# Performance work log

Measured on AMD Instinct MI355X. Metric: run time of the kernel, lower is better.

The kernel has to match this reference:

```python
import jax, jax.numpy as jnp
import numpy as np

# ---- static config (matches init_kwargs) ----
B, SX, SY, SZ = 1, 64, 64, 64
W = 32            # HIDDEN_DIM
L = 4             # num_fourier_layers
M1 = M2 = M3 = 8  # fourier modes per axis
PX = PY = PZ = 8  # domain padding
ALPHA = 0.05      # leaky relu slope
OUTC = 6


def conv3d(x, w, pad):
    # x: (B,C,D,H,W), w: (O,I,kd,kh,kw)
    return jax.lax.conv_general_dilated(
        x, w, window_strides=(1, 1, 1), padding=[(pad, pad)] * 3,
        dimension_numbers=('NCDHW', 'OIDHW', 'NCDHW'))


def pad1(x):
    # periodic=(0,0,0) -> zero pad 1 on every spatial side (matches ZeroPad3d chain)
    return jnp.pad(x, ((0, 0), (0, 0), (1, 1), (1, 1), (1, 1)))


def basic_block(x, w1, w2):
    # BasicBlock3D_Periodic with use_shortcut=False
    out = jax.nn.leaky_relu(conv3d(pad1(x), w1, 0), ALPHA)
    return conv3d(pad1(out), w2, 0)


def spec_apply(xft_slice, w):
    # xft_slice: complex (B,C,d1,d2,d3); w: (2C,2C,5,5,5)
    re_im = jnp.concatenate([xft_slice.real, xft_slice.imag], axis=1)  # (B,2C,...)
    out = conv3d(re_im, w, 2)                                          # (B,2C,...)
    b, c2, d1, d2, d3 = out.shape
    out = out.reshape(b, c2 // 2, 2, d1, d2, d3)
    return jax.lax.complex(out[:, :, 0], out[:, :, 1])


def spectral_conv(x, ws):
    # ws: (8, 2W, 2W, 5, 5, 5); mode-limited per-octant conv in frequency space
    b, c, n, m, l = x.shape
    xft = jnp.fft.rfftn(x, axes=(-3, -2, -1))  # (b,c,n,m,l//2+1) complex
    out = jnp.zeros((b, c, n, m, l // 2 + 1), dtype=xft.dtype)
    octs = [
        (slice(None, M1),  slice(None, M2)),
        (slice(n - M1, None), slice(None, M2)),
        (slice(None, M1),  slice(m - M2, None)),
        (slice(n - M1, None), slice(m - M2, None)),
        (slice(M1, n - M1), slice(None, M2)),
        (slice(None, M1),  slice(M2, m - M2)),
        (slice(M1, n - M1), slice(m - M2, None)),
        (slice(n - M1, None), slice(M2, m - M2)),
    ]
    for i, (s1, s2) in enumerate(octs):
        out = out.at[:, :, s1, s2, :M3].set(spec_apply(xft[:, :, s1, s2, :M3], ws[i]))
    return jnp.fft.irfftn(out, s=(n, m, l), axes=(-3, -2, -1))


def setup_inputs() -> dict:
    key = jax.random.key(0)
    ks = jax.random.split(key, 16)
    f32 = jnp.float32
    d = {
        'yeex': jax.random.normal(ks[0], (B, SX, SY, SZ), f32),
        'yeey': jax.random.normal(ks[1], (B, SX, SY, SZ), f32),
        'yeez': jax.random.normal(ks[2], (B, SX, SY, SZ), f32),
        'fc0_w': jax.random.normal(ks[3], (6, W), f32) * 0.1,
        'fc0_b': jax.random.normal(ks[4], (W,), f32) * 0.01,
        'spec_w': jax.random.normal(ks[5], (L, 8, 2 * W, 2 * W, 5, 5, 5), f32) * 0.02,
        'blk_w1': jax.random.normal(ks[6], (L, W, W, 3, 3, 3), f32) * 0.05,
        'blk_w2': jax.random.normal(ks[7], (L, W, W, 3, 3, 3), f32) * 0.05,
        'fc1_w': jax.random.normal(ks[8], (W, 128), f32) * 0.05,
        'fc1_b': jax.random.normal(ks[9], (128,), f32) * 0.01,
        'fc2_w': jax.random.normal(ks[10], (128, OUTC), f32) * 0.05,
        'fc2_b': jax.random.normal(ks[11], (OUTC,), f32) * 0.01,
    }
    return d


def reference(yeex, yeey, yeez, fc0_w, fc0_b, spec_w, blk_w1, blk_w2,
              fc1_w, fc1_b, fc2_w, fc2_b):
    b, sx, sy, sz = yeez.shape
    # normalized coordinate grid (3 channels), as in standard FNO get_grid
    gx = jnp.broadcast_to(jnp.linspace(0., 1., sx, dtype=yeex.dtype)[None, :, None, None], (b, sx, sy, sz))
    gy = jnp.broadcast_to(jnp.linspace(0., 1., sy, dtype=yeex.dtype)[None, None, :, None], (b, sx, sy, sz))
    gz = jnp.broadcast_to(jnp.linspace(0., 1., sz, dtype=yeex.dtype)[None, None, None, :], (b, sx, sy, sz))
    inp = jnp.stack([yeex, yeey, yeez, gx, gy, gz], axis=-1)  # (b,sx,sy,sz,6)

    x = inp @ fc0_w + fc0_b                      # lift: (b,sx,sy,sz,W)
    x = jnp.transpose(x, (0, 4, 1, 2, 3))        # (b,W,sx,sy,sz)
    x = jnp.pad(x, ((0, 0), (0, 0), (0, PX), (0, PY), (0, PZ)))

    for i in range(L):
        x1 = spectral_conv(x, spec_w[i])
        x2 = basic_block(x, blk_w1[i], blk_w2[i])
        x = x1 + x2 + x
        if i < L - 1:
            x = jax.nn.leaky_relu(x, ALPHA)

    x = x[:, :, :sx, :sy, :sz]                   # crop domain padding
    x = jnp.transpose(x, (0, 2, 3, 4, 1))        # (b,sx,sy,sz,W)
    x = jax.nn.leaky_relu(x @ fc1_w + fc1_b, ALPHA)
    return x @ fc2_w + fc2_b                     # (b,sx,sy,sz,OUTC)
```

## Files before the change

kernel.cpp:

```cpp
#include <hip/hip_runtime.h>
#include <math.h>

#define NS 72
#define NS2 (NS*NS)
#define NS3 (NS*NS*NS)
#define MZ 8
#define LALPHA 0.05f
#define CSCALE (1.0f/256.0f)

typedef _Float16 f16x8 __attribute__((ext_vector_type(8)));
typedef _Float16 f16x4 __attribute__((ext_vector_type(4)));
typedef float f32x4 __attribute__((ext_vector_type(4)));

__device__ __forceinline__ float leakyf(float v){ return v > 0.f ? v : LALPHA*v; }

__constant__ int c_RX0[8] = {0,64,0,64, 8,0,8,64};
__constant__ int c_RNX[8] = {8,8,8,8, 56,8,56,8};
__constant__ int c_RY0[8] = {0,0,64,64, 0,8,64,8};
__constant__ int c_RNY[8] = {8,8,8,8, 8,56,8,56};
__constant__ int c_Bbase[8] = {0,1728,3456,5184, 6912,15552,24192,32832};
__constant__ int c_BY[8]    = {12,12,12,12, 12,60,12,60};

__global__ void k_tw(float2* tw){
  int t = threadIdx.x;
  if (t < NS){
    double th = (2.0*M_PI/72.0)*(double)t;
    tw[t] = make_float2((float)cos(th), (float)sin(th));
  }
}

__global__ void k_fc0(const float* __restrict__ yx, const float* __restrict__ yy,
                      const float* __restrict__ yz, const float* __restrict__ w,
                      const float* __restrict__ b, float* __restrict__ X){
  int idx = blockIdx.x*256 + threadIdx.x;
  int z = idx % NS; int t = idx / NS; int y = t % NS; t /= NS; int x = t % NS; int c = t / NS;
  float v = 0.f;
  if (x < 64 && y < 64 && z < 64){
    int p = (x*64 + y)*64 + z;
    float i0 = yx[p], i1 = yy[p], i2 = yz[p];
    float gx = (float)x*(1.f/63.f), gy = (float)y*(1.f/63.f), gz = (float)z*(1.f/63.f);
    v = b[c] + i0*w[0*32+c] + i1*w[1*32+c] + i2*w[2*32+c]
             + gx*w[3*32+c] + gy*w[4*32+c] + gz*w[5*32+c];
  }
  X[idx] = v;
}

__global__ void k_zdft(const float* __restrict__ X, float2* __restrict__ A, const float2* __restrict__ tw){
  __shared__ float2 stw[NS];
  int tid = threadIdx.x;
  if (tid < NS) stw[tid] = tw[tid];
  __syncthreads();
  int f = blockIdx.x*256 + tid;
  const float* row = X + (size_t)f*NS;
  float ar[MZ], ai[MZ]; int tk[MZ];
  #pragma unroll
  for (int k=0;k<MZ;k++){ ar[k]=0.f; ai[k]=0.f; tk[k]=0; }
  for (int z=0; z<NS; z++){
    float v = row[z];
    #pragma unroll
    for (int k=0;k<MZ;k++){
      float2 w = stw[tk[k]];
      ar[k] += v*w.x;
      ai[k] -= v*w.y;
      tk[k] += k; if (tk[k] >= NS) tk[k] -= NS;
    }
  }
  float2* o = A + (size_t)f*MZ;
  #pragma unroll
  for (int k=0;k<MZ;k++) o[k] = make_float2(ar[k], ai[k]);
}

__global__ void k_ydft(const float2* __restrict__ A, float2* __restrict__ B, const float2* __restrict__ tw){
  __shared__ float2 stw[NS];
  int tid = threadIdx.x;
  if (tid < NS) stw[tid] = tw[tid];
  __syncthreads();
  int f = blockIdx.x*256 + tid;
  int ky = f % NS; int cx = f / NS;
  const float2* in = A + (size_t)cx*NS*MZ;
  float ar[MZ], ai[MZ];
  #pragma unroll
  for (int k=0;k<MZ;k++){ ar[k]=0.f; ai[k]=0.f; }
  int t = 0;
  for (int y=0;y<NS;y++){
    float2 w = stw[t]; t += ky; if (t>=NS) t-=NS;
    const float2* iy = in + y*MZ;
    #pragma unroll
    for (int k=0;k<MZ;k++){
      float2 v = iy[k];
      ar[k] += v.x*w.x + v.y*w.y;
      ai[k] += v.y*w.x - v.x*w.y;
    }
  }
  float2* o = B + (size_t)f*MZ;
  #pragma unroll
  for (int k=0;k<MZ;k++) o[k] = make_float2(ar[k], ai[k]);
}

__global__ void k_xdft(const float2* __restrict__ B, float2* __restrict__ C, const float2* __restrict__ tw){
  __shared__ float2 stw[NS];
  int tid = threadIdx.x;
  if (tid < NS) stw[tid] = tw[tid];
  __syncthreads();
  int f = blockIdx.x*256 + tid;
  int ky = f % NS; int t2 = f / NS; int kx = t2 % NS; int c = t2 / NS;
  const float2* in = B + ((size_t)c*NS2 + ky)*MZ;
  float ar[MZ], ai[MZ];
  #pragma unroll
  for (int k=0;k<MZ;k++){ ar[k]=0.f; ai[k]=0.f; }
  int t = 0;
  for (int x=0;x<NS;x++){
    float2 w = stw[t]; t += kx; if (t>=NS) t-=NS;
    const float2* ix = in + (size_t)x*NS*MZ;
    #pragma unroll
    for (int k=0;k<MZ;k++){
      float2 v = ix[k];
      ar[k] += v.x*w.x + v.y*w.y;
      ai[k] += v.y*w.x - v.x*w.y;
    }
  }
  float2* o = C + (size_t)f*MZ;
  #pragma unroll
  for (int k=0;k<MZ;k++) o[k] = make_float2(ar[k], ai[k]);
}

__global__ void k_wpackh(const float* __restrict__ W, _Float16* __restrict__ Ah){
  int e = blockIdx.x*256 + threadIdx.x;
  int i = e & 63; int o = (e>>6) & 63;
  int t2 = e >> 12; int tap = t2 % 125; int r = t2 / 125;
  const float* wr = W + (size_t)r*64*64*125;
  Ah[e] = (_Float16)wr[((size_t)(o*64 + (i&1)*32 + (i>>1)))*125 + tap];
}

__global__ void k_cpackh(const float2* __restrict__ C, _Float16* __restrict__ Bg){
  int g = blockIdx.x*256 + threadIdx.x;
  int ci = g & 31; int elem = g >> 5;
  int r = 0;
  #pragma unroll
  for (int k=1;k<8;k++) if (elem >= c_Bbase[k]) r = k;
  int el = elem - c_Bbase[r];
  int BY = c_BY[r];
  int q3 = el % 12; int tt = el / 12; int q2 = tt % BY; int q1 = tt / BY;
  int kxr = q1-2, kyr = q2-2, kzr = q3-2;
  float2 v = make_float2(0.f,0.f);
  if ((unsigned)kxr < (unsigned)c_RNX[r] && (unsigned)kyr < (unsigned)c_RNY[r] && (unsigned)kzr < 8u){
    v = C[(((size_t)ci*NS + (c_RX0[r]+kxr))*NS + (c_RY0[r]+kyr))*MZ + kzr];
  }
  _Float16* o = Bg + (size_t)elem*64 + 2*ci;
  o[0] = (_Float16)(v.x*CSCALE);
  o[1] = (_Float16)(v.y*CSCALE);
}

__global__ __launch_bounds__(64) void k_freqmfma(const _Float16* __restrict__ Ah,
                                                 const _Float16* __restrict__ Bg,
                                                 float* __restrict__ Pp){
  int gb = blockIdx.x;
  int ks = gb >> 8; int b = gb & 255;
  int r, til;
  if (b < 32){ r = b>>3; til = b&7; }
  else       { r = 4 + (b-32)/56; til = (b-32)%56; }
  int BY = c_BY[r];
  int q1, q2base;
  if (r==5 || r==7){ q1 = 2 + til/7; q2base = 2 + (til%7)*8; }
  else             { q1 = 2 + til;   q2base = 2; }
  int lane = threadIdx.x;
  int l15 = lane & 15, kg = lane >> 4;
  int q2l = q2base + (l15>>3), q3l = 2 + (l15&7);
  const _Float16* Ar = Ah + (size_t)r*125*4096;
  const _Float16* Br = Bg + (size_t)c_Bbase[r]*64;
  int lb = q2l*12 + q3l;
  f32x4 acc[4][4];
  f32x4 zz = {0.f,0.f,0.f,0.f};
  #pragma unroll
  for (int m=0;m<4;m++)
    #pragma unroll
    for (int n=0;n<4;n++) acc[m][n] = zz;
  int t0 = ks*16;
  int t1 = t0+16 < 125 ? t0+16 : 125;
  for (int tt=t0; tt<t1; tt++){
    int td = tt/25; int rm = tt - td*25; int th = rm/5; int tz = rm - th*5;
    const _Float16* At = Ar + tt*4096;
    f16x8 a[4][2];
    #pragma unroll
    for (int mt=0;mt<4;mt++){
      a[mt][0] = *(const f16x8*)(At + (mt*16+l15)*64 + kg*8);
      a[mt][1] = *(const f16x8*)(At + (mt*16+l15)*64 + 32 + kg*8);
    }
    int ebase = (q1 + td - 2)*BY*12 + lb + (th-2)*12 + (tz-2);
    f16x8 bf[4][2];
    #pragma unroll
    for (int nt=0;nt<4;nt++){
      const _Float16* bp = Br + (size_t)(ebase + nt*24)*64 + kg*8;
      bf[nt][0] = *(const f16x8*)(bp);
      bf[nt][1] = *(const f16x8*)(bp + 32);
    }
    #pragma unroll
    for (int mt=0;mt<4;mt++)
      #pragma unroll
      for (int nt=0;nt<4;nt++){
        acc[mt][nt] = __builtin_amdgcn_mfma_f32_16x16x32_f16(a[mt][0], bf[nt][0], acc[mt][nt],0,0,0);
        acc[mt][nt] = __builtin_amdgcn_mfma_f32_16x16x32_f16(a[mt][1], bf[nt][1], acc[mt][nt],0,0,0);
      }
  }
  float* base = Pp + (((size_t)ks*256 + b)*64 + lane)*64;
  #pragma unroll
  for (int mt=0;mt<4;mt++)
    #pragma unroll
    for (int nt=0;nt<4;nt++)
      *(f32x4*)(base + mt*16 + nt*4) = acc[mt][nt];
}

__global__ void k_fred(const float* __restrict__ Pp, float* __restrict__ Df){
  int t = blockIdx.x*256 + threadIdx.x;
  int mtnt = t & 15; int lane = (t>>4) & 63; int b = t >> 10;
  int mt = mtnt >> 2, nt = mtnt & 3;
  int r, til;
  if (b < 32){ r = b>>3; til = b&7; }
  else       { r = 4 + (b-32)/56; til = (b-32)%56; }
  int x0 = c_RX0[r], y0 = c_RY0[r];
  int q1, q2base;
  if (r==5 || r==7){ q1 = 2 + til/7; q2base = 2 + (til%7)*8; }
  else             { q1 = 2 + til;   q2base = 2; }
  int l15 = lane & 15, kg = lane >> 4;
  int q2l = q2base + (l15>>3), q3l = 2 + (l15&7);
  f32x4 s = {0.f,0.f,0.f,0.f};
  #pragma unroll
  for (int ks=0;ks<8;ks++){
    s += *(const f32x4*)(Pp + (((size_t)ks*256 + b)*64 + lane)*64 + mtnt*4);
  }
  int kx = x0 + q1 - 2;
  int kz = q3l - 2;
  int ky = y0 + q2l + nt*2 - 2;
  #pragma unroll
  for (int rg=0;rg<4;rg++){
    int o = mt*16 + kg*4 + rg;
    int co = o >> 1, reim = o & 1;
    Df[((((size_t)co*NS + kx)*NS + ky)*MZ + kz)*2 + reim] = s[rg]*256.0f;
  }
}

__global__ void k_invx(const float2* __restrict__ D, float2* __restrict__ E, const float2* __restrict__ tw){
  __shared__ float2 stw[NS];
  int tid = threadIdx.x;
  if (tid < NS) stw[tid] = tw[tid];
  __syncthreads();
  int f = blockIdx.x*256 + tid;
  int ky = f % NS; int t2 = f / NS; int x = t2 % NS; int c = t2 / NS;
  const float2* in = D + ((size_t)c*NS2 + ky)*MZ;
  float ar[MZ], ai[MZ];
  #pragma unroll
  for (int k=0;k<MZ;k++){ ar[k]=0.f; ai[k]=0.f; }
  int t = 0;
  for (int kx=0;kx<NS;kx++){
    float2 w = stw[t]; t += x; if (t>=NS) t-=NS;
    const float2* ix = in + (size_t)kx*NS*MZ;
    #pragma unroll
    for (int k=0;k<MZ;k++){
      float2 v = ix[k];
      ar[k] += v.x*w.x - v.y*w.y;
      ai[k] += v.x*w.y + v.y*w.x;
    }
  }
  float2* o = E + (size_t)f*MZ;
  #pragma unroll
  for (int k=0;k<MZ;k++) o[k] = make_float2(ar[k]*(1.f/72.f), ai[k]*(1.f/72.f));
}

__global__ void k_invyz(const float2* __restrict__ E, float* __restrict__ X1, const float2* __restrict__ tw){
  __shared__ float2 stw[NS];
  int tid = threadIdx.x;
  if (tid < NS) stw[tid] = tw[tid];
  __syncthreads();
  int f = blockIdx.x*256 + tid;
  int y = f % NS; int t2 = f / NS; int x = t2 % NS; int c = t2 / NS;
  const float2* in = E + ((size_t)c*NS + x)*NS*MZ;
  float ar[MZ], ai[MZ];
  #pragma unroll
  for (int k=0;k<MZ;k++){ ar[k]=0.f; ai[k]=0.f; }
  int t = 0;
  for (int ky=0;ky<NS;ky++){
    float2 w = stw[t]; t += y; if (t>=NS) t-=NS;
    const float2* ik = in + ky*MZ;
    #pragma unroll
    for (int k=0;k<MZ;k++){
      float2 v = ik[k];
      ar[k] += v.x*w.x - v.y*w.y;
      ai[k] += v.x*w.y + v.y*w.x;
    }
  }
  const float scale = 1.f/(72.f*72.f);
  float* o = X1 + (size_t)f*NS;
  int tk[MZ];
  #pragma unroll
  for (int k=0;k<MZ;k++) tk[k]=0;
  for (int z=0; z<NS; z++){
    float acc = ar[0];
    #pragma unroll
    for (int k=1;k<MZ;k++){
      float2 w = stw[tk[k]];
      acc += 2.f*(ar[k]*w.x - ai[k]*w.y);
      tk[k] += k; if (tk[k] >= NS) tk[k] -= NS;
    }
    o[z] = acc*scale;
  }
}


__global__ void k_wcvt2(const float* __restrict__ w1, const float* __restrict__ w2,
                        _Float16* __restrict__ WhA, _Float16* __restrict__ WhB){
  int e = blockIdx.x*256 + threadIdx.x;
  int h = e >= 27648; int e2 = e - (h ? 27648 : 0);
  int tap = e2 >> 10; int co = (e2>>5)&31; int ci = e2&31;
  const float* w = h ? w2 : w1;
  _Float16* o = h ? WhB : WhA;
  o[e2] = (_Float16)w[(co*32+ci)*27 + tap];
}

__global__ void k_cvt16(const float* __restrict__ Xf, _Float16* __restrict__ Xg){
  int b = blockIdx.x;
  int tid = threadIdx.x;
  if (b >= 1458){
    _Float16* g = (b==1458) ? (Xg - 4096) : (Xg + (size_t)NS3*32);
    f16x8 zz = {0,0,0,0,0,0,0,0};
    f16x8* gp = (f16x8*)g;
    gp[tid] = zz; gp[tid+256] = zz;
    return;
  }
  int p = b*256 + tid;
  f16x8 o0,o1,o2,o3;
  #pragma unroll
  for (int c=0;c<8;c++){
    o0[c] = (_Float16)Xf[(size_t)c*NS3 + p];
    o1[c] = (_Float16)Xf[(size_t)(c+8)*NS3 + p];
    o2[c] = (_Float16)Xf[(size_t)(c+16)*NS3 + p];
    o3[c] = (_Float16)Xf[(size_t)(c+24)*NS3 + p];
  }
  f16x8* op = (f16x8*)(Xg + (size_t)p*32);
  op[0]=o0; op[1]=o1; op[2]=o2; op[3]=o3;
}

__global__ void k_zgH(_Float16* __restrict__ Hg){
  int e = blockIdx.x*256 + threadIdx.x;
  _Float16* g = (e < 512) ? (Hg - 4096 + e*8)
                          : (Hg + (size_t)NS3*32 + (size_t)(e-512)*8);
  f16x8 zz = {0,0,0,0,0,0,0,0};
  *(f16x8*)g = zz;
}

__global__ __launch_bounds__(256) void k_convm(const _Float16* __restrict__ Xg,
    const _Float16* __restrict__ Wh, float* __restrict__ OUT, _Float16* __restrict__ OUTH,
    const float* __restrict__ X1, const float* __restrict__ Xres,
    int mode2, int do_leaky){
  int tid = threadIdx.x;
  int orig = blockIdx.x;
  int xcd = orig & 7, loc = orig >> 3;
  int wg = (xcd < 2 ? xcd*183 : 366 + (xcd-2)*182) + loc;
  int j = wg*4 + (tid>>6);
  int slab = j/81, nb = j - slab*81;
  int q0 = nb*64;
  int lane = tid & 63;
  int l15 = lane & 15, kg = lane >> 4;
  f32x4 acc[2][4];
  f32x4 zz = {0.f,0.f,0.f,0.f};
  #pragma unroll
  for (int a=0;a<2;a++)
    #pragma unroll
    for (int b=0;b<4;b++) acc[a][b] = zz;
  for (int dx=0; dx<3; dx++){
    int xx = slab + dx - 1;
    if ((unsigned)xx >= 72u) continue;
    const _Float16* Xrow = Xg + ((size_t)xx*5184 + q0)*32;
    #pragma unroll
    for (int t9=0; t9<9; t9++){
      int tap = dx*9 + t9;
      int off = ((t9/3)-1)*72 + (t9%3) - 1;
      f16x8 a0 = *(const f16x8*)(Wh + ((tap*32 + l15)*32 + kg*8));
      f16x8 a1 = *(const f16x8*)(Wh + ((tap*32 + 16 + l15)*32 + kg*8));
      const _Float16* bbase = Xrow + (off + l15)*32 + kg*8;
      f16x8 b0 = *(const f16x8*)(bbase);
      f16x8 b1 = *(const f16x8*)(bbase + 512);
      f16x8 b2 = *(const f16x8*)(bbase + 1024);
      f16x8 b3 = *(const f16x8*)(bbase + 1536);
      acc[0][0] = __builtin_amdgcn_mfma_f32_16x16x32_f16(a0,b0,acc[0][0],0,0,0);
      acc[0][1] = __builtin_amdgcn_mfma_f32_16x16x32_f16(a0,b1,acc[0][1],0,0,0);
      acc[0][2] = __builtin_amdgcn_mfma_f32_16x16x32_f16(a0,b2,acc[0][2],0,0,0);
      acc[0][3] = __builtin_amdgcn_mfma_f32_16x16x32_f16(a0,b3,acc[0][3],0,0,0);
      acc[1][0] = __builtin_amdgcn_mfma_f32_16x16x32_f16(a1,b0,acc[1][0],0,0,0);
      acc[1][1] = __builtin_amdgcn_mfma_f32_16x16x32_f16(a1,b1,acc[1][1],0,0,0);
      acc[1][2] = __builtin_amdgcn_mfma_f32_16x16x32_f16(a1,b2,acc[1][2],0,0,0);
      acc[1][3] = __builtin_amdgcn_mfma_f32_16x16x32_f16(a1,b3,acc[1][3],0,0,0);
    }
  }
  if (mode2){
    #pragma unroll
    for (int nt=0; nt<4; nt++){
      int q = q0 + nt*16 + l15;
      int y = q/72, z = q - y*72;
      bool edge = (y==0)||(y==71)||(z==0)||(z==71);
      #pragma unroll
      for (int c2=0;c2<2;c2++){
        #pragma unroll
        for (int r=0;r<4;r++){
          int co = c2*16 + kg*4 + r;
          size_t idx = (size_t)co*NS3 + (size_t)slab*5184 + q;
          float v = acc[c2][nt][r];
          if (!edge){
            v += X1[idx] + Xres[idx];
            if (do_leaky) v = leakyf(v);
          }
          OUT[idx] = v;
        }
      }
    }
  } else {
    #pragma unroll
    for (int nt=0; nt<4; nt++){
      int q = q0 + nt*16 + l15;
      int y = q/72, z = q - y*72;
      bool edge = (y==0)||(y==71)||(z==0)||(z==71);
      _Float16* hp = OUTH + ((size_t)slab*5184 + q)*32 + kg*4;
      #pragma unroll
      for (int c2=0;c2<2;c2++){
        f32x4 av = acc[c2][nt];
        f16x4 hv;
        #pragma unroll
        for (int r=0;r<4;r++){
          float v = av[r];
          if (!edge) v = leakyf(v);
          hv[r] = (_Float16)v;
        }
        *(f16x4*)(hp + c2*16) = hv;
      }
    }
  }
}

__global__ void k_corrH(_Float16* __restrict__ H, const _Float16* __restrict__ Xg,
                        const _Float16* __restrict__ Wh){
  int t = blockIdx.x*256 + threadIdx.x;
  int co = t & 31; int t2 = t >> 5;
  int e = t2 % 284; int x = t2 / 284;
  int y, z;
  if (e < 72){ y = 0; z = e; }
  else if (e < 144){ y = 71; z = e - 72; }
  else if (e < 214){ z = 0; y = e - 143; }
  else { z = 71; y = e - 213; }
  int q = y*72 + z;
  float corr = 0.f;
  for (int tap=0; tap<27; tap++){
    int dx = tap/9, rr = tap%9, dy = rr/3, dz = rr%3;
    int xx = x + dx - 1;
    if ((unsigned)xx >= 72u) continue;
    int yy = y + dy - 1, zz = z + dz - 1;
    if ((unsigned)yy < 72u && (unsigned)zz < 72u) continue;
    int lin = (xx*5184 + q + (dy-1)*72 + (dz-1))*32;
    const _Float16* V = Xg + lin;
    const _Float16* Wr = Wh + (tap*32 + co)*32;
    float s = 0.f;
    #pragma unroll
    for (int ci=0; ci<32; ci++) s += (float)V[ci]*(float)Wr[ci];
    corr += s;
  }
  size_t idx = ((size_t)x*5184 + q)*32 + co;
  float v = (float)H[idx] - corr;
  v = leakyf(v);
  H[idx] = (_Float16)v;
}

__global__ void k_corr(float* __restrict__ OUT, const _Float16* __restrict__ Xg,
                       const _Float16* __restrict__ Wh, const float* __restrict__ X1,
                       const float* __restrict__ Xres, int mode2, int do_leaky){
  int t = blockIdx.x*256 + threadIdx.x;
  int co = t & 31; int t2 = t >> 5;
  int e = t2 % 284; int x = t2 / 284;
  int y, z;
  if (e < 72){ y = 0; z = e; }
  else if (e < 144){ y = 71; z = e - 72; }
  else if (e < 214){ z = 0; y = e - 143; }
  else { z = 71; y = e - 213; }
  int q = y*72 + z;
  float corr = 0.f;
  for (int tap=0; tap<27; tap++){
    int dx = tap/9, rr = tap%9, dy = rr/3, dz = rr%3;
    int xx = x + dx - 1;
    if ((unsigned)xx >= 72u) continue;
    int yy = y + dy - 1, zz = z + dz - 1;
    if ((unsigned)yy < 72u && (unsigned)zz < 72u) continue;
    int lin = (xx*5184 + q + (dy-1)*72 + (dz-1))*32;
    const _Float16* V = Xg + lin;
    const _Float16* Wr = Wh + (tap*32 + co)*32;
    float s = 0.f;
    #pragma unroll
    for (int ci=0; ci<32; ci++) s += (float)V[ci]*(float)Wr[ci];
    corr += s;
  }
  size_t idx = (size_t)co*NS3 + (size_t)x*5184 + q;
  float v = OUT[idx] - corr;
  if (mode2) v += X1[idx] + Xres[idx];
  if (do_leaky) v = leakyf(v);
  OUT[idx] = v;
}

__global__ void k_head(const float* __restrict__ X, const float* __restrict__ w1, const float* __restrict__ b1,
                       const float* __restrict__ w2, const float* __restrict__ b2, float* __restrict__ out){
  __shared__ float s1[32*128];
  __shared__ float sb1[128];
  __shared__ float s2[128*6];
  __shared__ float sb2[6];
  int tid = threadIdx.x;
  for (int e=tid;e<4096;e+=256) s1[e]=w1[e];
  if (tid<128) sb1[tid]=b1[tid];
  for (int e=tid;e<768;e+=256) s2[e]=w2[e];
  if (tid<6) sb2[tid]=b2[tid];
  __syncthreads();
  int p = blockIdx.x*256 + tid;
  int z = p % 64; int t = p / 64; int y = t % 64; int x = t / 64;
  size_t q = ((size_t)x*NS + y)*NS + z;
  float xin[32];
  #pragma unroll
  for (int c=0;c<32;c++) xin[c] = X[(size_t)c*NS3 + q];
  float acc[6];
  #pragma unroll
  for (int o=0;o<6;o++) acc[o]=sb2[o];
  for (int j=0;j<128;j++){
    float h = sb1[j];
    #pragma unroll
    for (int c=0;c<32;c++) h += xin[c]*s1[c*128+j];
    h = leakyf(h);
    #pragma unroll
    for (int o=0;o<6;o++) acc[o] += h*s2[j*6+o];
  }
  float* O = out + (size_t)p*6;
  #pragma unroll
  for (int o=0;o<6;o++) O[o]=acc[o];
}

extern "C" void kernel_launch(void* const* d_in, const int* in_sizes, int n_in,
                              void* d_out, int out_size, void* d_ws, size_t ws_size,
                              hipStream_t stream) {
  const float* yeex = (const float*)d_in[0];
  const float* yeey = (const float*)d_in[1];
  const float* yeez = (const float*)d_in[2];
  const float* fc0w = (const float*)d_in[3];
  const float* fc0b = (const float*)d_in[4];
  const float* specw= (const float*)d_in[5];
  const float* bw1  = (const float*)d_in[6];
  const float* bw2  = (const float*)d_in[7];
  const float* fc1w = (const float*)d_in[8];
  const float* fc1b = (const float*)d_in[9];
  const float* fc2w = (const float*)d_in[10];
  const float* fc2b = (const float*)d_in[11];
  float* out = (float*)d_out;
  float* ws  = (float*)d_ws;

  float*  P0 = ws;
  float*  X1 = ws + 11943936;
  float*  P2 = ws + 23887872;
  float2* A  = (float2*)(ws + 35831808);
  float2* B  = (float2*)(ws + 41140224);
  float2* Cf = (float2*)(ws + 46448640);
  float2* Df = (float2*)(ws + 51757056);
  float2* TW = (float2*)(ws + 57065472);
  _Float16* Ah = (_Float16*)A;
  _Float16* Bg = (_Float16*)B;
  float*    Pp = X1;
  _Float16* XhG = (_Float16*)(ws + 35831808) + 4096;
  _Float16* HhG = (_Float16*)(ws + 41807872) + 4096;
  _Float16* WhA = (_Float16*)(ws + 47783936);
  _Float16* WhB = (_Float16*)(ws + 47797760);

  float* curX = P0; float* curY = P2;

  k_tw<<<1,128,0,stream>>>(TW);
  k_fc0<<<46656,256,0,stream>>>(yeex,yeey,yeez,fc0w,fc0b,curX);
  for (int i=0;i<4;i++){
    k_zdft<<<648,256,0,stream>>>(curX, A, TW);
    k_ydft<<<648,256,0,stream>>>(A, B, TW);
    k_xdft<<<648,256,0,stream>>>(B, Cf, TW);
    k_wpackh<<<16000,256,0,stream>>>(specw + (size_t)i*8*64*64*125, Ah);
    k_cpackh<<<5184,256,0,stream>>>(Cf, Bg);
    hipMemsetAsync(Df, 0, (size_t)1327104*8, stream);
    k_freqmfma<<<2048,64,0,stream>>>(Ah, Bg, Pp);
    k_fred<<<1024,256,0,stream>>>(Pp, (float*)Df);
    k_invx<<<648,256,0,stream>>>(Df, A, TW);
    k_invyz<<<648,256,0,stream>>>(A, X1, TW);
    k_wcvt2<<<216,256,0,stream>>>(bw1 + (size_t)i*27648, bw2 + (size_t)i*27648, WhA, WhB);
    k_cvt16<<<1460,256,0,stream>>>(curX, XhG);
    k_zgH<<<4,256,0,stream>>>(HhG);
    k_convm<<<1458,256,0,stream>>>(XhG, WhA, nullptr, HhG, nullptr, nullptr, 0, 1);
    k_corrH<<<2556,256,0,stream>>>(HhG, XhG, WhA);
    k_convm<<<1458,256,0,stream>>>(HhG, WhB, curY, nullptr, X1, curX, 1, (i<3)?1:0);
    k_corr<<<2556,256,0,stream>>>(curY, HhG, WhB, X1, curX, 1, (i<3)?1:0);
    float* tmp = curX; curX = curY; curY = tmp;
  }
  k_head<<<1024,256,0,stream>>>(curX, fc1w, fc1b, fc2w, fc2b, out);
}
```

Measured before the change: 2.557 ms.

## Prune x-DFT to retained modes, store spectral output and residual in fp16, retile head

The x-axis DFT now computes only the frequency rows that the mode-limited spectral weights later read, split across two threads per output (four z-modes each). The spectral-branch output X1 is written as fp16, and the residual is read from the existing fp16 channel-last copy of the input instead of the fp32 tensor, which cuts epilogue memory traffic in the conv kernels. The head kernel handles two points per thread, reads transposed fc1 weights as float4 from LDS, and launches half as many blocks. Storing the spectral output and residual in fp16 lowers precision on the residual path, and the residual reads become strided across channels.

```diff
diff --git a/kernel.cpp b/kernel.cpp
--- a/kernel.cpp
+++ b/kernel.cpp
@@ -97,31 +97,38 @@
   for (int k=0;k<MZ;k++) o[k] = make_float2(ar[k], ai[k]);
 }
 
-__global__ void k_xdft(const float2* __restrict__ B, float2* __restrict__ C, const float2* __restrict__ tw){
+__global__ void k_xdftL(const float2* __restrict__ B, float2* __restrict__ C, const float2* __restrict__ tw){
   __shared__ float2 stw[NS];
   int tid = threadIdx.x;
   if (tid < NS) stw[tid] = tw[tid];
   __syncthreads();
-  int f = blockIdx.x*256 + tid;
-  int ky = f % NS; int t2 = f / NS; int kx = t2 % NS; int c = t2 / NS;
-  const float2* in = B + ((size_t)c*NS2 + ky)*MZ;
-  float ar[MZ], ai[MZ];
-  #pragma unroll
-  for (int k=0;k<MZ;k++){ ar[k]=0.f; ai[k]=0.f; }
-  int t = 0;
+  int t = blockIdx.x*256 + tid;
+  int h = t & 1; int t2 = t >> 1;
+  int c = t2 >> 11; int l = t2 & 2047;
+  int kx, ky;
+  if (l < 576){ ky = l & 7; kx = l >> 3; }
+  else if (l < 1152){ int e = l - 576; ky = 64 + (e & 7); kx = e >> 3; }
+  else { int e = l - 1152; int kyi = e >> 4; int kxi = e & 15;
+         ky = 8 + kyi; kx = (kxi < 8) ? kxi : 56 + kxi; }
+  int k0 = h*4;
+  const float2* in = B + ((size_t)c*NS2 + ky)*MZ + k0;
+  float ar[4], ai[4];
+  #pragma unroll
+  for (int k=0;k<4;k++){ ar[k]=0.f; ai[k]=0.f; }
+  int tt = 0;
   for (int x=0;x<NS;x++){
-    float2 w = stw[t]; t += kx; if (t>=NS) t-=NS;
+    float2 w = stw[tt]; tt += kx; if (tt>=NS) tt-=NS;
     const float2* ix = in + (size_t)x*NS*MZ;
     #pragma unroll
-    for (int k=0;k<MZ;k++){
+    for (int k=0;k<4;k++){
       float2 v = ix[k];
       ar[k] += v.x*w.x + v.y*w.y;
       ai[k] += v.y*w.x - v.x*w.y;
     }
   }
-  float2* o = C + (size_t)f*MZ;
-  #pragma unroll
-  for (int k=0;k<MZ;k++) o[k] = make_float2(ar[k], ai[k]);
+  float2* o = C + (((size_t)c*NS + kx)*NS + ky)*MZ + k0;
+  #pragma unroll
+  for (int k=0;k<4;k++) o[k] = make_float2(ar[k], ai[k]);
 }
 
 __global__ void k_wpackh(const float* __restrict__ W, _Float16* __restrict__ Ah){
@@ -266,7 +273,7 @@
   for (int k=0;k<MZ;k++) o[k] = make_float2(ar[k]*(1.f/72.f), ai[k]*(1.f/72.f));
 }
 
-__global__ void k_invyz(const float2* __restrict__ E, float* __restrict__ X1, const float2* __restrict__ tw){
+__global__ void k_invyz(const float2* __restrict__ E, _Float16* __restrict__ X1h, const float2* __restrict__ tw){
   __shared__ float2 stw[NS];
   int tid = threadIdx.x;
   if (tid < NS) stw[tid] = tw[tid];
@@ -289,7 +296,7 @@
     }
   }
   const float scale = 1.f/(72.f*72.f);
-  float* o = X1 + (size_t)f*NS;
+  _Float16* o = X1h + (size_t)f*NS;
   int tk[MZ];
   #pragma unroll
   for (int k=0;k<MZ;k++) tk[k]=0;
@@ -301,7 +308,7 @@
       acc += 2.f*(ar[k]*w.x - ai[k]*w.y);
       tk[k] += k; if (tk[k] >= NS) tk[k] -= NS;
     }
-    o[z] = acc*scale;
+    o[z] = (_Float16)(acc*scale);
   }
 }
 
@@ -349,7 +356,7 @@
 
 __global__ __launch_bounds__(256) void k_convm(const _Float16* __restrict__ Xg,
     const _Float16* __restrict__ Wh, float* __restrict__ OUT, _Float16* __restrict__ OUTH,
-    const float* __restrict__ X1, const float* __restrict__ Xres,
+    const _Float16* __restrict__ X1h, const _Float16* __restrict__ XresH,
     int mode2, int do_leaky){
   int tid = threadIdx.x;
   int orig = blockIdx.x;
@@ -405,7 +412,7 @@
           size_t idx = (size_t)co*NS3 + (size_t)slab*5184 + q;
           float v = acc[c2][nt][r];
           if (!edge){
-            v += X1[idx] + Xres[idx];
+            v += (float)X1h[idx] + (float)XresH[((size_t)slab*5184 + q)*32 + co];
             if (do_leaky) v = leakyf(v);
           }
           OUT[idx] = v;
@@ -468,8 +475,8 @@
 }
 
 __global__ void k_corr(float* __restrict__ OUT, const _Float16* __restrict__ Xg,
-                       const _Float16* __restrict__ Wh, const float* __restrict__ X1,
-                       const float* __restrict__ Xres, int mode2, int do_leaky){
+                       const _Float16* __restrict__ Wh, const _Float16* __restrict__ X1h,
+                       const _Float16* __restrict__ XresH, int mode2, int do_leaky){
   int t = blockIdx.x*256 + threadIdx.x;
   int co = t & 31; int t2 = t >> 5;
   int e = t2 % 284; int x = t2 / 284;
@@ -496,43 +503,60 @@
   }
   size_t idx = (size_t)co*NS3 + (size_t)x*5184 + q;
   float v = OUT[idx] - corr;
-  if (mode2) v += X1[idx] + Xres[idx];
+  if (mode2) v += (float)X1h[idx] + (float)XresH[((size_t)x*5184 + q)*32 + co];
   if (do_leaky) v = leakyf(v);
   OUT[idx] = v;
 }
 
 __global__ void k_head(const float* __restrict__ X, const float* __restrict__ w1, const float* __restrict__ b1,
                        const float* __restrict__ w2, const float* __restrict__ b2, float* __restrict__ out){
-  __shared__ float s1[32*128];
+  __shared__ float s1t[32*128];
   __shared__ float sb1[128];
   __shared__ float s2[128*6];
   __shared__ float sb2[6];
   int tid = threadIdx.x;
-  for (int e=tid;e<4096;e+=256) s1[e]=w1[e];
+  for (int e=tid;e<4096;e+=256){ int j=e>>5, c=e&31; s1t[e]=w1[c*128+j]; }
   if (tid<128) sb1[tid]=b1[tid];
   for (int e=tid;e<768;e+=256) s2[e]=w2[e];
   if (tid<6) sb2[tid]=b2[tid];
   __syncthreads();
-  int p = blockIdx.x*256 + tid;
-  int z = p % 64; int t = p / 64; int y = t % 64; int x = t / 64;
-  size_t q = ((size_t)x*NS + y)*NS + z;
-  float xin[32];
-  #pragma unroll
-  for (int c=0;c<32;c++) xin[c] = X[(size_t)c*NS3 + q];
-  float acc[6];
-  #pragma unroll
-  for (int o=0;o<6;o++) acc[o]=sb2[o];
+  int p0 = blockIdx.x*256 + tid;
+  float xin[2][32];
+  float acc[2][6];
+  #pragma unroll
+  for (int vv=0; vv<2; vv++){
+    int p = p0 + vv*131072;
+    int z = p % 64; int t = p / 64; int y = t % 64; int x = t / 64;
+    size_t q = ((size_t)x*NS + y)*NS + z;
+    #pragma unroll
+    for (int c=0;c<32;c++) xin[vv][c] = X[(size_t)c*NS3 + q];
+    #pragma unroll
+    for (int o=0;o<6;o++) acc[vv][o]=sb2[o];
+  }
   for (int j=0;j<128;j++){
-    float h = sb1[j];
-    #pragma unroll
-    for (int c=0;c<32;c++) h += xin[c]*s1[c*128+j];
-    h = leakyf(h);
-    #pragma unroll
-    for (int o=0;o<6;o++) acc[o] += h*s2[j*6+o];
-  }
-  float* O = out + (size_t)p*6;
-  #pragma unroll
-  for (int o=0;o<6;o++) O[o]=acc[o];
+    const float4* wj = (const float4*)(s1t + j*32);
+    float h0 = sb1[j], h1 = h0;
+    #pragma unroll
+    for (int c4=0;c4<8;c4++){
+      float4 w = wj[c4];
+      h0 += xin[0][c4*4+0]*w.x + xin[0][c4*4+1]*w.y + xin[0][c4*4+2]*w.z + xin[0][c4*4+3]*w.w;
+      h1 += xin[1][c4*4+0]*w.x + xin[1][c4*4+1]*w.y + xin[1][c4*4+2]*w.z + xin[1][c4*4+3]*w.w;
+    }
+    h0 = leakyf(h0); h1 = leakyf(h1);
+    const float* s2j = s2 + j*6;
+    #pragma unroll
+    for (int o=0;o<6;o++){
+      float wv = s2j[o];
+      acc[0][o] += h0*wv;
+      acc[1][o] += h1*wv;
+    }
+  }
+  #pragma unroll
+  for (int vv=0; vv<2; vv++){
+    float* O = out + (size_t)(p0 + vv*131072)*6;
+    #pragma unroll
+    for (int o=0;o<6;o++) O[o]=acc[vv][o];
+  }
 }
 
 extern "C" void kernel_launch(void* const* d_in, const int* in_sizes, int n_in,
@@ -554,7 +578,7 @@
   float* ws  = (float*)d_ws;
 
   float*  P0 = ws;
-  float*  X1 = ws + 11943936;
+  float*  X1s = ws + 11943936;
   float*  P2 = ws + 23887872;
   float2* A  = (float2*)(ws + 35831808);
   float2* B  = (float2*)(ws + 41140224);
@@ -563,7 +587,8 @@
   float2* TW = (float2*)(ws + 57065472);
   _Float16* Ah = (_Float16*)A;
   _Float16* Bg = (_Float16*)B;
-  float*    Pp = X1;
+  float*    Pp = X1s;
+  _Float16* X1h = (_Float16*)X1s;
   _Float16* XhG = (_Float16*)(ws + 35831808) + 4096;
   _Float16* HhG = (_Float16*)(ws + 41807872) + 4096;
   _Float16* WhA = (_Float16*)(ws + 47783936);
@@ -576,22 +601,22 @@
   for (int i=0;i<4;i++){
     k_zdft<<<648,256,0,stream>>>(curX, A, TW);
     k_ydft<<<648,256,0,stream>>>(A, B, TW);
-    k_xdft<<<648,256,0,stream>>>(B, Cf, TW);
+    k_xdftL<<<512,256,0,stream>>>(B, Cf, TW);
     k_wpackh<<<16000,256,0,stream>>>(specw + (size_t)i*8*64*64*125, Ah);
     k_cpackh<<<5184,256,0,stream>>>(Cf, Bg);
     hipMemsetAsync(Df, 0, (size_t)1327104*8, stream);
     k_freqmfma<<<2048,64,0,stream>>>(Ah, Bg, Pp);
     k_fred<<<1024,256,0,stream>>>(Pp, (float*)Df);
     k_invx<<<648,256,0,stream>>>(Df, A, TW);
-    k_invyz<<<648,256,0,stream>>>(A, X1, TW);
+    k_invyz<<<648,256,0,stream>>>(A, X1h, TW);
     k_wcvt2<<<216,256,0,stream>>>(bw1 + (size_t)i*27648, bw2 + (size_t)i*27648, WhA, WhB);
     k_cvt16<<<1460,256,0,stream>>>(curX, XhG);
     k_zgH<<<4,256,0,stream>>>(HhG);
     k_convm<<<1458,256,0,stream>>>(XhG, WhA, nullptr, HhG, nullptr, nullptr, 0, 1);
     k_corrH<<<2556,256,0,stream>>>(HhG, XhG, WhA);
-    k_convm<<<1458,256,0,stream>>>(HhG, WhB, curY, nullptr, X1, curX, 1, (i<3)?1:0);
-    k_corr<<<2556,256,0,stream>>>(curY, HhG, WhB, X1, curX, 1, (i<3)?1:0);
+    k_convm<<<1458,256,0,stream>>>(HhG, WhB, curY, nullptr, X1h, XhG, 1, (i<3)?1:0);
+    k_corr<<<2556,256,0,stream>>>(curY, HhG, WhB, X1h, XhG, 1, (i<3)?1:0);
     float* tmp = curX; curX = curY; curY = tmp;
   }
-  k_head<<<1024,256,0,stream>>>(curX, fc1w, fc1b, fc2w, fc2b, out);
-}
+  k_head<<<512,256,0,stream>>>(curX, fc1w, fc1b, fc2w, fc2b, out);
+}
```

Measured after the change: 2.401 ms. 1.06x faster.
